# Optimization experiments

Hardware: AMD Instinct MI355X
Metric: run time of the kernel (lower is better)

## Reference

```python
import jax, jax.numpy as jnp
import numpy as np


def conv1x1(x, w, b):
    # x: [B,Ci,H,W], w: [Co,Ci,1,1], b: [Co]
    return jnp.einsum('bihw,oi->bohw', x, w[:, :, 0, 0]) + b[None, :, None, None]


def guide_nn(x, w1, b1, w2, b2):
    h = jax.nn.relu(conv1x1(x, w1, b1))
    return jnp.tanh(conv1x1(h, w2, b2))


def trilinear_slice(grid, gx, gy, gz):
    # grid: [B,C,D,Gh,Gw]; gx,gy,gz: [B,H,W] in ~[-1,1]
    B, C, D, Gh, Gw = grid.shape
    fx = jnp.clip((gx + 1.0) * 0.5 * (Gw - 1), 0.0, Gw - 1)
    fy = jnp.clip((gy + 1.0) * 0.5 * (Gh - 1), 0.0, Gh - 1)
    fz = jnp.clip((gz + 1.0) * 0.5 * (D - 1), 0.0, D - 1)
    x0 = jnp.floor(fx).astype(jnp.int32); x1 = jnp.minimum(x0 + 1, Gw - 1)
    y0 = jnp.floor(fy).astype(jnp.int32); y1 = jnp.minimum(y0 + 1, Gh - 1)
    z0 = jnp.floor(fz).astype(jnp.int32); z1 = jnp.minimum(z0 + 1, D - 1)
    wx = (fx - x0)[:, None]; wy = (fy - y0)[:, None]; wz = (fz - z0)[:, None]

    gather = jax.vmap(lambda g, zi, yi, xi: g[:, zi, yi, xi])  # -> [B,C,H,W]

    out = (
        gather(grid, z0, y0, x0) * (1 - wz) * (1 - wy) * (1 - wx)
        + gather(grid, z0, y0, x1) * (1 - wz) * (1 - wy) * wx
        + gather(grid, z0, y1, x0) * (1 - wz) * wy * (1 - wx)
        + gather(grid, z0, y1, x1) * (1 - wz) * wy * wx
        + gather(grid, z1, y0, x0) * wz * (1 - wy) * (1 - wx)
        + gather(grid, z1, y0, x1) * wz * (1 - wy) * wx
        + gather(grid, z1, y1, x0) * wz * wy * (1 - wx)
        + gather(grid, z1, y1, x1) * wz * wy * wx
    )
    return out


def slicing(grid, guide):
    # guide: [B,1,H,W] (single-channel context map)
    B, c, H, W = guide.shape
    x = (jnp.arange(W, dtype=guide.dtype) - W / 2) / (W / 2)
    y = (jnp.arange(H, dtype=guide.dtype) - H / 2) / (H / 2)
    yy, xx = jnp.meshgrid(y, x, indexing='ij')
    gx = jnp.broadcast_to(xx[None], (B, H, W))
    gy = jnp.broadcast_to(yy[None], (B, H, W))
    gz = guide[:, 0]
    return trilinear_slice(grid, gx, gy, gz)


def apply_coefficent(x, coeff):
    # x: [B,Ci,H,W]; coeff: [B,Co,Ci+1,H,W] -> per-pixel affine
    ci = x.shape[1]
    return jnp.einsum('boihw,bihw->bohw', coeff[:, :, :ci], x) + coeff[:, :, ci]


def setup_inputs() -> dict:
    key = jax.random.key(0)
    ks = jax.random.split(key, 12)
    B, H, W = 8, 512, 512
    D, Gh, Gw = 8, 16, 16
    inp = {
        'src': jax.random.uniform(ks[0], (B, 3, H, W), jnp.float32),
        'grid1': jax.random.normal(ks[1], (B, 32, D, Gh, Gw), jnp.float32),
        'grid2': jax.random.normal(ks[2], (B, 27, D, Gh, Gw), jnp.float32),
        'w1': jax.random.normal(ks[3], (16, 3, 1, 1), jnp.float32) * 0.1,
        'b1': jnp.zeros((16,), jnp.float32),
        'w2': jax.random.normal(ks[4], (1, 16, 1, 1), jnp.float32) * 0.1,
        'b2': jnp.zeros((1,), jnp.float32),
        'w3': jax.random.normal(ks[5], (16, 8, 1, 1), jnp.float32) * 0.1,
        'b3': jnp.zeros((16,), jnp.float32),
        'w4': jax.random.normal(ks[6], (1, 16, 1, 1), jnp.float32) * 0.1,
        'b4': jnp.zeros((1,), jnp.float32),
    }
    return inp


def reference(src, grid1, grid2, w1, b1, w2, b2, w3, b3, w4, b4):
    B, _, H, W = src.shape
    context_map = guide_nn(src, w1, b1, w2, b2)            # [B,1,H,W]
    coeff1 = slicing(grid1, context_map)                    # [B,32,H,W]
    coeff1_split = jnp.transpose(coeff1.reshape(B, 4, 8, H, W), (0, 2, 1, 3, 4))  # [B,8,4,H,W]
    hidden = jax.nn.relu(apply_coefficent(src, coeff1_split))  # [B,8,H,W]
    context_map2 = guide_nn(hidden, w3, b3, w4, b4)         # [B,1,H,W]
    coeff2 = slicing(grid2, context_map2)                   # [B,27,H,W]
    coeff2_split = jnp.transpose(coeff2.reshape(B, 9, 3, H, W), (0, 2, 1, 3, 4))  # [B,3,9,H,W]
    out = apply_coefficent(hidden, coeff2_split)            # [B,3,H,W]
    return out
```

## Files before the change

kernel.cpp:

```cpp
#include <hip/hip_runtime.h>
#include <math.h>

#define BATCH 8
#define IMH 512
#define IMW 512
#define HWSZ (IMH * IMW)
#define CH 32
#define CPADH 40
#define L_CELLS (16 * 8)
#define LSLOTH (L_CELLS * CPADH)

typedef _Float16 h1;
typedef _Float16 h2 __attribute__((ext_vector_type(2)));

union V16 {
    uint4 u;
    h2 h[4];
};

__device__ __forceinline__ float fast_tanh(float x) {
    float e = __expf(2.0f * x);
    return fmaf(-2.0f, __builtin_amdgcn_rcpf(e + 1.0f), 1.0f);
}
__device__ __forceinline__ unsigned packh(float a, float b) {
    h2 v;
    v[0] = (h1)a;
    v[1] = (h1)b;
    return __builtin_bit_cast(unsigned, v);
}
__device__ __forceinline__ h2 ash2(unsigned u) { return __builtin_bit_cast(h2, u); }
__device__ __forceinline__ h2 pkmax0(h2 v) { return __builtin_elementwise_max(v, (h2)(h1)0.0f); }


__global__ __launch_bounds__(256) void transpose_both(const float* __restrict__ g1,
                                                      const float* __restrict__ g2,
                                                      h1* __restrict__ t1,
                                                      h1* __restrict__ t2,
                                                      unsigned* __restrict__ wpk,
                                                      const float* __restrict__ w1,
                                                      const float* __restrict__ b1,
                                                      const float* __restrict__ w2,
                                                      const float* __restrict__ w3,
                                                      const float* __restrict__ b3,
                                                      const float* __restrict__ w4) {
    int idx = blockIdx.x * 256 + threadIdx.x;
    if (idx < 524288) {
        int x = idx & 15, y = (idx >> 4) & 15, z = (idx >> 8) & 7;
        int c = (idx >> 11) & 31, b = idx >> 16;
        t1[((((b * 16 + y) * 16 + x) * 8 + z) << 5) + c] = (h1)g1[idx];
    } else if (idx < 966656) {
        int j = idx - 524288;
        int x = j & 15, y = (j >> 4) & 15, z = (j >> 8) & 7;
        int r = j >> 11;
        int c = r % 27, b = r / 27;
        t2[((((b * 16 + y) * 16 + x) * 8 + z) << 5) + c] = (h1)g2[j];
    } else {
        int k = idx - 966656;
        int cell = k / 5, p = k - cell * 5;
        t2[(cell << 5) + 27 + p] = (h1)0.0f;
    }
    if (blockIdx.x == 4095) {
        int t = threadIdx.x;
        if (t < 24) {
            int i = t >> 3, n = t & 7;
            wpk[t] = packh(w1[2 * n * 3 + i], w1[(2 * n + 1) * 3 + i]);
        } else if (t < 32) {
            int n = t - 24;
            wpk[t] = packh(b1[2 * n], b1[2 * n + 1]);
        } else if (t < 40) {
            int n = t - 32;
            wpk[t] = packh(w2[2 * n], w2[2 * n + 1]);
        } else if (t < 104) {
            int k = t - 40;
            int n = k >> 3, i = k & 7;
            wpk[t] = packh(w3[2 * n * 8 + i], w3[(2 * n + 1) * 8 + i]);
        } else if (t < 112) {
            int n = t - 104;
            wpk[t] = packh(w4[2 * n], w4[2 * n + 1]);
        } else if (t < 120) {
            int n = t - 112;
            wpk[t] = packh(b3[2 * n], b3[2 * n + 1]);
        }
    }
}

template <bool TR>
__global__ __launch_bounds__(256, 4) void fused6(
    const float* __restrict__ src,
    const void* __restrict__ g1p,
    const void* __restrict__ g2p,
    const unsigned* __restrict__ wpk,
    const float* __restrict__ w1, const float* __restrict__ b1,
    const float* __restrict__ w2, const float* __restrict__ b2,
    const float* __restrict__ w3, const float* __restrict__ b3,
    const float* __restrict__ w4, const float* __restrict__ b4,
    float* __restrict__ out) {
    __shared__ __align__(16) h1 L1h[LSLOTH];
    __shared__ __align__(16) h1 L2h[LSLOTH];

    int tid = threadIdx.x;
    int h = blockIdx.x & 511;
    int b = blockIdx.x >> 9;

    float fy = (float)h * (15.0f / 512.0f);
    int y0 = (int)fy;
    float wy = fy - (float)y0;

    const float* sbase = src + (size_t)b * 3 * HWSZ + (size_t)h * IMW;
    float sA0 = sbase[tid],       sA1 = sbase[HWSZ + tid],       sA2 = sbase[2 * HWSZ + tid];
    float sB0 = sbase[tid + 256], sB1 = sbase[HWSZ + tid + 256], sB2 = sbase[2 * HWSZ + tid + 256];

    if (TR) {
        h2 wyh = (h2)(h1)wy;
        const uint4* p1 = (const uint4*)g1p + ((size_t)b * 16 + y0) * 512;
        const uint4* p2 = (const uint4*)g2p + ((size_t)b * 16 + y0) * 512;
#pragma unroll
        for (int t = tid; t < 512; t += 256) {
            int g = t & 3, cell = t >> 2;
            V16 v0, v1, r0;
            v0.u = p1[t];
            v1.u = p1[t + 512];
#pragma unroll
            for (int k = 0; k < 4; ++k) r0.h[k] = v0.h[k] + (v1.h[k] - v0.h[k]) * wyh;
            *(uint4*)&L1h[cell * CPADH + 8 * g] = r0.u;
            V16 u0, u1, r1;
            u0.u = p2[t];
            u1.u = p2[t + 512];
#pragma unroll
            for (int k = 0; k < 4; ++k) r1.h[k] = u0.h[k] + (u1.h[k] - u0.h[k]) * wyh;
            *(uint4*)&L2h[cell * CPADH + 8 * g] = r1.u;
        }
    } else {
        const float* g1f = (const float*)g1p;
        const float* g2f = (const float*)g2p;
        for (int t = tid; t < L_CELLS * CH; t += 256) {
            int c = t & 31, cell = t >> 5;
            int z = cell & 7, xj = cell >> 3;
            size_t o0 = ((((size_t)b * 32 + c) * 8 + z) * 16 + y0) * 16 + xj;
            float v0 = g1f[o0], v1 = g1f[o0 + 16];
            L1h[cell * CPADH + c] = (h1)fmaf(wy, v1 - v0, v0);
        }
        for (int t = tid; t < L_CELLS * CH; t += 256) {
            int c = t & 31, cell = t >> 5;
            int z = cell & 7, xj = cell >> 3;
            float v = 0.0f;
            if (c < 27) {
                size_t o0 = ((((size_t)b * 27 + c) * 8 + z) * 16 + y0) * 16 + xj;
                v = fmaf(wy, g2f[o0 + 16] - g2f[o0], g2f[o0]);
            }
            L2h[cell * CPADH + c] = (h1)v;
        }
    }
    __syncthreads();

    float* obase = out + (size_t)b * 3 * HWSZ + (size_t)h * IMW;
#pragma unroll 2
    for (int p = 0; p < 2; ++p) {
        int w = tid + (p << 8);
        float s0 = p ? sB0 : sA0;
        float s1 = p ? sB1 : sA1;
        float s2 = p ? sB2 : sA2;

        float acc;
        h2 s0h, s1h, s2h;
        if constexpr (TR) {
            s0h = (h2)(h1)s0;
            s1h = (h2)(h1)s1;
            s2h = (h2)(h1)s2;
            h2 A;
#pragma unroll
            for (int n = 0; n < 8; ++n) {
                h2 t = ash2(wpk[24 + n]);
                t += s0h * ash2(wpk[n]);
                t += s1h * ash2(wpk[8 + n]);
                t += s2h * ash2(wpk[16 + n]);
                t = pkmax0(t);
                if (n == 0) A = t * ash2(wpk[32]);
                else        A += t * ash2(wpk[32 + n]);
            }
            acc = b2[0] + (float)A[0] + (float)A[1];
        } else {
            acc = b2[0];
#pragma unroll
            for (int j = 0; j < 16; ++j) {
                float t = fmaf(w1[j * 3 + 0], s0,
                          fmaf(w1[j * 3 + 1], s1,
                          fmaf(w1[j * 3 + 2], s2, b1[j])));
                acc = fmaf(w2[j], fmaxf(t, 0.0f), acc);
            }
        }
        float fz = fmaf(fast_tanh(acc), 3.5f, 3.5f);
        fz = fminf(fmaxf(fz, 0.0f), 7.0f);
        int z0 = min((int)fz, 6);
        float wz = fz - (float)z0;

        float fx = (float)w * (15.0f / 512.0f);
        int x0 = (int)fx;
        float wx = fx - (float)x0;
        int a00 = (x0 * 8 + z0) * CPADH;

        float w11v = wx * wz;
        float w10v = wx - w11v;
        float w01v = wz - w11v;
        float w00v = 1.0f - wx - wz + w11v;
        h2 W00 = (h2)(h1)w00v, W01 = (h2)(h1)w01v, W10 = (h2)(h1)w10v, W11 = (h2)(h1)w11v;

        const uint4* p00 = (const uint4*)&L1h[a00];
        const uint4* p01 = (const uint4*)&L1h[a00 + CPADH];
        const uint4* p10 = (const uint4*)&L1h[a00 + 8 * CPADH];
        const uint4* p11 = (const uint4*)&L1h[a00 + 9 * CPADH];
        h2 c1h[16];
#pragma unroll
        for (int j = 0; j < 4; ++j) {
            V16 A, B, C, D;
            A.u = p00[j];
            B.u = p01[j];
            C.u = p10[j];
            D.u = p11[j];
#pragma unroll
            for (int k = 0; k < 4; ++k)
                c1h[j * 4 + k] = A.h[k] * W00 + B.h[k] * W01 + C.h[k] * W10 + D.h[k] * W11;
        }

        h2 hidh[4];
        float hidf[8];
        if constexpr (TR) {
#pragma unroll
            for (int n = 0; n < 4; ++n) {
                h2 t = c1h[12 + n];
                t += c1h[n] * s0h;
                t += c1h[4 + n] * s1h;
                t += c1h[8 + n] * s2h;
                hidh[n] = pkmax0(t);
                hidf[2 * n]     = (float)hidh[n][0];
                hidf[2 * n + 1] = (float)hidh[n][1];
            }
        } else {
#pragma unroll
            for (int o = 0; o < 8; ++o) {
                float t = fmaf((float)c1h[o >> 1][o & 1], s0,
                          fmaf((float)c1h[(8 + o) >> 1][o & 1], s1,
                          fmaf((float)c1h[(16 + o) >> 1][o & 1], s2,
                               (float)c1h[(24 + o) >> 1][o & 1])));
                hidf[o] = fmaxf(t, 0.0f);
            }
        }

        float acc2;
        if constexpr (TR) {
            h2 hs[8];
#pragma unroll
            for (int n = 0; n < 4; ++n) {
                hs[2 * n]     = (h2)hidh[n][0];
                hs[2 * n + 1] = (h2)hidh[n][1];
            }
            h2 A;
#pragma unroll
            for (int n = 0; n < 8; ++n) {
                h2 t = ash2(wpk[112 + n]);
#pragma unroll
                for (int i = 0; i < 8; ++i) t += hs[i] * ash2(wpk[40 + n * 8 + i]);
                t = pkmax0(t);
                if (n == 0) A = t * ash2(wpk[104]);
                else        A += t * ash2(wpk[104 + n]);
            }
            acc2 = b4[0] + (float)A[0] + (float)A[1];
        } else {
            acc2 = b4[0];
#pragma unroll
            for (int j = 0; j < 16; ++j) {
                float t = b3[j];
#pragma unroll
                for (int i = 0; i < 8; ++i) t = fmaf(w3[j * 8 + i], hidf[i], t);
                acc2 = fmaf(w4[j], fmaxf(t, 0.0f), acc2);
            }
        }
        float fz2 = fmaf(fast_tanh(acc2), 3.5f, 3.5f);
        fz2 = fminf(fmaxf(fz2, 0.0f), 7.0f);
        int z0b = min((int)fz2, 6);
        float wz2 = fz2 - (float)z0b;

        int a00b = (x0 * 8 + z0b) * CPADH;
        float u11 = wx * wz2;
        float u10 = wx - u11;
        float u01 = wz2 - u11;
        float u00 = 1.0f - wx - wz2 + u11;
        h2 U00 = (h2)(h1)u00, U01 = (h2)(h1)u01, U10 = (h2)(h1)u10, U11 = (h2)(h1)u11;

        const uint4* q00 = (const uint4*)&L2h[a00b];
        const uint4* q01 = (const uint4*)&L2h[a00b + CPADH];
        const uint4* q10 = (const uint4*)&L2h[a00b + 8 * CPADH];
        const uint4* q11 = (const uint4*)&L2h[a00b + 9 * CPADH];
        h2 c2h[14];
#pragma unroll
        for (int j = 0; j < 4; ++j) {
            V16 A, B, C, D;
            A.u = q00[j];
            B.u = q01[j];
            C.u = q10[j];
            D.u = q11[j];
#pragma unroll
            for (int k = 0; k < 4; ++k) {
                int m = j * 4 + k;
                if (m < 14)
                    c2h[m] = A.h[k] * U00 + B.h[k] * U01 + C.h[k] * U10 + D.h[k] * U11;
            }
        }

#pragma unroll
        for (int o = 0; o < 3; ++o) {
            float t = (float)c2h[(24 + o) >> 1][(24 + o) & 1];
#pragma unroll
            for (int i = 0; i < 8; ++i) {
                int c = i * 3 + o;
                t = fmaf((float)c2h[c >> 1][c & 1], hidf[i], t);
            }
            obase[(size_t)o * HWSZ + w] = t;
        }
    }
}

extern "C" void kernel_launch(void* const* d_in, const int* in_sizes, int n_in,
                              void* d_out, int out_size, void* d_ws, size_t ws_size,
                              hipStream_t stream) {
    const float* src   = (const float*)d_in[0];
    const float* grid1 = (const float*)d_in[1];
    const float* grid2 = (const float*)d_in[2];
    const float* w1 = (const float*)d_in[3];
    const float* b1 = (const float*)d_in[4];
    const float* w2 = (const float*)d_in[5];
    const float* b2 = (const float*)d_in[6];
    const float* w3 = (const float*)d_in[7];
    const float* b3 = (const float*)d_in[8];
    const float* w4 = (const float*)d_in[9];
    const float* b4 = (const float*)d_in[10];
    float* out = (float*)d_out;

    const size_t t_elems = (size_t)BATCH * 2048 * CH;
    const size_t ws_needed = 2 * t_elems * sizeof(h1) + 512;

    const int nblk = BATCH * IMH;

    if (ws_size >= ws_needed) {
        h1* t1 = (h1*)d_ws;
        h1* t2 = t1 + t_elems;
        unsigned* wpk = (unsigned*)(t2 + t_elems);
        transpose_both<<<4096, 256, 0, stream>>>(grid1, grid2, t1, t2, wpk,
                                                 w1, b1, w2, w3, b3, w4);
        fused6<true><<<nblk, 256, 0, stream>>>(
            src, t1, t2, wpk, w1, b1, w2, b2, w3, b3, w4, b4, out);
    } else {
        fused6<false><<<nblk, 256, 0, stream>>>(
            src, grid1, grid2, nullptr, w1, b1, w2, b2, w3, b3, w4, b4, out);
    }
}
```

Before: 121.9 us.

## Split each image row across two blocks with half-width grid staging

Each block now handles half a row (256 pixels, one per thread) and stages only the 9 x-cells of the y-interpolated bilateral grid that its half needs, instead of all 16. This halves LDS use per block, which allows a higher occupancy target in launch bounds, and doubles the grid size. The second-slice load now reads only the 27 used channels (3 uint4 plus one uint2 per corner). The hidf conversion moves after the second guide MLP. In exchange, the grid staging work for each row is partly repeated, since about 18 cells are loaded per row instead of 16, and each block does less work to amortize its setup.

Result: no change. 123.3 us (+1.1%).

```diff
diff --git a/kernel.cpp b/kernel.cpp
--- a/kernel.cpp
+++ b/kernel.cpp
@@ -7,8 +7,10 @@
 #define HWSZ (IMH * IMW)
 #define CH 32
 #define CPADH 40
-#define L_CELLS (16 * 8)
+#define XCELLS 9
+#define L_CELLS (XCELLS * 8)
 #define LSLOTH (L_CELLS * CPADH)
+#define NCHUNK (L_CELLS * 4)
 
 typedef _Float16 h1;
 typedef _Float16 h2 __attribute__((ext_vector_type(2)));
@@ -16,6 +18,10 @@
 union V16 {
     uint4 u;
     h2 h[4];
+};
+union V8 {
+    uint2 u;
+    h2 h[2];
 };
 
 __device__ __forceinline__ float fast_tanh(float x) {
@@ -85,7 +91,7 @@
 }
 
 template <bool TR>
-__global__ __launch_bounds__(256, 4) void fused6(
+__global__ __launch_bounds__(256, 8) void fused8(
     const float* __restrict__ src,
     const void* __restrict__ g1p,
     const void* __restrict__ g2p,
@@ -99,23 +105,27 @@
     __shared__ __align__(16) h1 L2h[LSLOTH];
 
     int tid = threadIdx.x;
-    int h = blockIdx.x & 511;
-    int b = blockIdx.x >> 9;
+    int gid = blockIdx.x;
+    int half = gid & 1;
+    int h = (gid >> 1) & 511;
+    int b = gid >> 10;
+    int xlo = half ? 7 : 0;
+    int w = (half << 8) + tid;
 
     float fy = (float)h * (15.0f / 512.0f);
     int y0 = (int)fy;
     float wy = fy - (float)y0;
 
     const float* sbase = src + (size_t)b * 3 * HWSZ + (size_t)h * IMW;
-    float sA0 = sbase[tid],       sA1 = sbase[HWSZ + tid],       sA2 = sbase[2 * HWSZ + tid];
-    float sB0 = sbase[tid + 256], sB1 = sbase[HWSZ + tid + 256], sB2 = sbase[2 * HWSZ + tid + 256];
+    float s0 = sbase[w];
+    float s1 = sbase[HWSZ + w];
+    float s2 = sbase[2 * HWSZ + w];
 
     if (TR) {
         h2 wyh = (h2)(h1)wy;
-        const uint4* p1 = (const uint4*)g1p + ((size_t)b * 16 + y0) * 512;
-        const uint4* p2 = (const uint4*)g2p + ((size_t)b * 16 + y0) * 512;
-#pragma unroll
-        for (int t = tid; t < 512; t += 256) {
+        const uint4* p1 = (const uint4*)g1p + ((size_t)b * 16 + y0) * 512 + xlo * 32;
+        const uint4* p2 = (const uint4*)g2p + ((size_t)b * 16 + y0) * 512 + xlo * 32;
+        for (int t = tid; t < NCHUNK; t += 256) {
             int g = t & 3, cell = t >> 2;
             V16 v0, v1, r0;
             v0.u = p1[t];
@@ -123,6 +133,9 @@
 #pragma unroll
             for (int k = 0; k < 4; ++k) r0.h[k] = v0.h[k] + (v1.h[k] - v0.h[k]) * wyh;
             *(uint4*)&L1h[cell * CPADH + 8 * g] = r0.u;
+        }
+        for (int t = tid; t < NCHUNK; t += 256) {
+            int g = t & 3, cell = t >> 2;
             V16 u0, u1, r1;
             u0.u = p2[t];
             u1.u = p2[t + 512];
@@ -135,14 +148,14 @@
         const float* g2f = (const float*)g2p;
         for (int t = tid; t < L_CELLS * CH; t += 256) {
             int c = t & 31, cell = t >> 5;
-            int z = cell & 7, xj = cell >> 3;
+            int z = cell & 7, xj = xlo + (cell >> 3);
             size_t o0 = ((((size_t)b * 32 + c) * 8 + z) * 16 + y0) * 16 + xj;
             float v0 = g1f[o0], v1 = g1f[o0 + 16];
             L1h[cell * CPADH + c] = (h1)fmaf(wy, v1 - v0, v0);
         }
         for (int t = tid; t < L_CELLS * CH; t += 256) {
             int c = t & 31, cell = t >> 5;
-            int z = cell & 7, xj = cell >> 3;
+            int z = cell & 7, xj = xlo + (cell >> 3);
             float v = 0.0f;
             if (c < 27) {
                 size_t o0 = ((((size_t)b * 27 + c) * 8 + z) * 16 + y0) * 16 + xj;
@@ -154,169 +167,172 @@
     __syncthreads();
 
     float* obase = out + (size_t)b * 3 * HWSZ + (size_t)h * IMW;
-#pragma unroll 2
-    for (int p = 0; p < 2; ++p) {
-        int w = tid + (p << 8);
-        float s0 = p ? sB0 : sA0;
-        float s1 = p ? sB1 : sA1;
-        float s2 = p ? sB2 : sA2;
-
-        float acc;
-        h2 s0h, s1h, s2h;
-        if constexpr (TR) {
-            s0h = (h2)(h1)s0;
-            s1h = (h2)(h1)s1;
-            s2h = (h2)(h1)s2;
-            h2 A;
-#pragma unroll
-            for (int n = 0; n < 8; ++n) {
-                h2 t = ash2(wpk[24 + n]);
-                t += s0h * ash2(wpk[n]);
-                t += s1h * ash2(wpk[8 + n]);
-                t += s2h * ash2(wpk[16 + n]);
-                t = pkmax0(t);
-                if (n == 0) A = t * ash2(wpk[32]);
-                else        A += t * ash2(wpk[32 + n]);
-            }
-            acc = b2[0] + (float)A[0] + (float)A[1];
-        } else {
-            acc = b2[0];
-#pragma unroll
-            for (int j = 0; j < 16; ++j) {
-                float t = fmaf(w1[j * 3 + 0], s0,
-                          fmaf(w1[j * 3 + 1], s1,
-                          fmaf(w1[j * 3 + 2], s2, b1[j])));
-                acc = fmaf(w2[j], fmaxf(t, 0.0f), acc);
-            }
-        }
-        float fz = fmaf(fast_tanh(acc), 3.5f, 3.5f);
-        fz = fminf(fmaxf(fz, 0.0f), 7.0f);
-        int z0 = min((int)fz, 6);
-        float wz = fz - (float)z0;
-
-        float fx = (float)w * (15.0f / 512.0f);
-        int x0 = (int)fx;
-        float wx = fx - (float)x0;
-        int a00 = (x0 * 8 + z0) * CPADH;
-
-        float w11v = wx * wz;
-        float w10v = wx - w11v;
-        float w01v = wz - w11v;
-        float w00v = 1.0f - wx - wz + w11v;
-        h2 W00 = (h2)(h1)w00v, W01 = (h2)(h1)w01v, W10 = (h2)(h1)w10v, W11 = (h2)(h1)w11v;
-
-        const uint4* p00 = (const uint4*)&L1h[a00];
-        const uint4* p01 = (const uint4*)&L1h[a00 + CPADH];
-        const uint4* p10 = (const uint4*)&L1h[a00 + 8 * CPADH];
-        const uint4* p11 = (const uint4*)&L1h[a00 + 9 * CPADH];
-        h2 c1h[16];
-#pragma unroll
-        for (int j = 0; j < 4; ++j) {
-            V16 A, B, C, D;
-            A.u = p00[j];
-            B.u = p01[j];
-            C.u = p10[j];
-            D.u = p11[j];
-#pragma unroll
-            for (int k = 0; k < 4; ++k)
-                c1h[j * 4 + k] = A.h[k] * W00 + B.h[k] * W01 + C.h[k] * W10 + D.h[k] * W11;
-        }
-
-        h2 hidh[4];
-        float hidf[8];
-        if constexpr (TR) {
-#pragma unroll
-            for (int n = 0; n < 4; ++n) {
-                h2 t = c1h[12 + n];
-                t += c1h[n] * s0h;
-                t += c1h[4 + n] * s1h;
-                t += c1h[8 + n] * s2h;
-                hidh[n] = pkmax0(t);
-                hidf[2 * n]     = (float)hidh[n][0];
-                hidf[2 * n + 1] = (float)hidh[n][1];
-            }
-        } else {
-#pragma unroll
-            for (int o = 0; o < 8; ++o) {
-                float t = fmaf((float)c1h[o >> 1][o & 1], s0,
-                          fmaf((float)c1h[(8 + o) >> 1][o & 1], s1,
-                          fmaf((float)c1h[(16 + o) >> 1][o & 1], s2,
-                               (float)c1h[(24 + o) >> 1][o & 1])));
-                hidf[o] = fmaxf(t, 0.0f);
-            }
-        }
-
-        float acc2;
-        if constexpr (TR) {
-            h2 hs[8];
-#pragma unroll
-            for (int n = 0; n < 4; ++n) {
-                hs[2 * n]     = (h2)hidh[n][0];
-                hs[2 * n + 1] = (h2)hidh[n][1];
-            }
-            h2 A;
-#pragma unroll
-            for (int n = 0; n < 8; ++n) {
-                h2 t = ash2(wpk[112 + n]);
-#pragma unroll
-                for (int i = 0; i < 8; ++i) t += hs[i] * ash2(wpk[40 + n * 8 + i]);
-                t = pkmax0(t);
-                if (n == 0) A = t * ash2(wpk[104]);
-                else        A += t * ash2(wpk[104 + n]);
-            }
-            acc2 = b4[0] + (float)A[0] + (float)A[1];
-        } else {
-            acc2 = b4[0];
-#pragma unroll
-            for (int j = 0; j < 16; ++j) {
-                float t = b3[j];
-#pragma unroll
-                for (int i = 0; i < 8; ++i) t = fmaf(w3[j * 8 + i], hidf[i], t);
-                acc2 = fmaf(w4[j], fmaxf(t, 0.0f), acc2);
-            }
-        }
-        float fz2 = fmaf(fast_tanh(acc2), 3.5f, 3.5f);
-        fz2 = fminf(fmaxf(fz2, 0.0f), 7.0f);
-        int z0b = min((int)fz2, 6);
-        float wz2 = fz2 - (float)z0b;
-
-        int a00b = (x0 * 8 + z0b) * CPADH;
-        float u11 = wx * wz2;
-        float u10 = wx - u11;
-        float u01 = wz2 - u11;
-        float u00 = 1.0f - wx - wz2 + u11;
-        h2 U00 = (h2)(h1)u00, U01 = (h2)(h1)u01, U10 = (h2)(h1)u10, U11 = (h2)(h1)u11;
-
-        const uint4* q00 = (const uint4*)&L2h[a00b];
-        const uint4* q01 = (const uint4*)&L2h[a00b + CPADH];
-        const uint4* q10 = (const uint4*)&L2h[a00b + 8 * CPADH];
-        const uint4* q11 = (const uint4*)&L2h[a00b + 9 * CPADH];
-        h2 c2h[14];
-#pragma unroll
-        for (int j = 0; j < 4; ++j) {
-            V16 A, B, C, D;
-            A.u = q00[j];
-            B.u = q01[j];
-            C.u = q10[j];
-            D.u = q11[j];
-#pragma unroll
-            for (int k = 0; k < 4; ++k) {
-                int m = j * 4 + k;
-                if (m < 14)
-                    c2h[m] = A.h[k] * U00 + B.h[k] * U01 + C.h[k] * U10 + D.h[k] * U11;
-            }
-        }
-
-#pragma unroll
-        for (int o = 0; o < 3; ++o) {
-            float t = (float)c2h[(24 + o) >> 1][(24 + o) & 1];
-#pragma unroll
-            for (int i = 0; i < 8; ++i) {
-                int c = i * 3 + o;
-                t = fmaf((float)c2h[c >> 1][c & 1], hidf[i], t);
-            }
-            obase[(size_t)o * HWSZ + w] = t;
-        }
+
+    float acc;
+    h2 s0h, s1h, s2h;
+    if constexpr (TR) {
+        s0h = (h2)(h1)s0;
+        s1h = (h2)(h1)s1;
+        s2h = (h2)(h1)s2;
+        h2 A;
+#pragma unroll
+        for (int n = 0; n < 8; ++n) {
+            h2 t = ash2(wpk[24 + n]);
+            t += s0h * ash2(wpk[n]);
+            t += s1h * ash2(wpk[8 + n]);
+            t += s2h * ash2(wpk[16 + n]);
+            t = pkmax0(t);
+            if (n == 0) A = t * ash2(wpk[32]);
+            else        A += t * ash2(wpk[32 + n]);
+        }
+        acc = b2[0] + (float)A[0] + (float)A[1];
+    } else {
+        acc = b2[0];
+#pragma unroll
+        for (int j = 0; j < 16; ++j) {
+            float t = fmaf(w1[j * 3 + 0], s0,
+                      fmaf(w1[j * 3 + 1], s1,
+                      fmaf(w1[j * 3 + 2], s2, b1[j])));
+            acc = fmaf(w2[j], fmaxf(t, 0.0f), acc);
+        }
+    }
+    float fz = fmaf(fast_tanh(acc), 3.5f, 3.5f);
+    fz = fminf(fmaxf(fz, 0.0f), 7.0f);
+    int z0 = min((int)fz, 6);
+    float wz = fz - (float)z0;
+
+    float fx = (float)w * (15.0f / 512.0f);
+    int x0 = (int)fx;
+    float wx = fx - (float)x0;
+    int a00 = ((x0 - xlo) * 8 + z0) * CPADH;
+
+    float w11v = wx * wz;
+    float w10v = wx - w11v;
+    float w01v = wz - w11v;
+    float w00v = 1.0f - wx - wz + w11v;
+    h2 W00 = (h2)(h1)w00v, W01 = (h2)(h1)w01v, W10 = (h2)(h1)w10v, W11 = (h2)(h1)w11v;
+
+    const uint4* p00 = (const uint4*)&L1h[a00];
+    const uint4* p01 = (const uint4*)&L1h[a00 + CPADH];
+    const uint4* p10 = (const uint4*)&L1h[a00 + 8 * CPADH];
+    const uint4* p11 = (const uint4*)&L1h[a00 + 9 * CPADH];
+    h2 c1h[16];
+#pragma unroll
+    for (int j = 0; j < 4; ++j) {
+        V16 A, B, C, D;
+        A.u = p00[j];
+        B.u = p01[j];
+        C.u = p10[j];
+        D.u = p11[j];
+#pragma unroll
+        for (int k = 0; k < 4; ++k)
+            c1h[j * 4 + k] = A.h[k] * W00 + B.h[k] * W01 + C.h[k] * W10 + D.h[k] * W11;
+    }
+
+    h2 hidh[4];
+    float hidf[8];
+    if constexpr (TR) {
+#pragma unroll
+        for (int n = 0; n < 4; ++n) {
+            h2 t = c1h[12 + n];
+            t += c1h[n] * s0h;
+            t += c1h[4 + n] * s1h;
+            t += c1h[8 + n] * s2h;
+            hidh[n] = pkmax0(t);
+        }
+    } else {
+#pragma unroll
+        for (int o = 0; o < 8; ++o) {
+            float t = fmaf((float)c1h[o >> 1][o & 1], s0,
+                      fmaf((float)c1h[(8 + o) >> 1][o & 1], s1,
+                      fmaf((float)c1h[(16 + o) >> 1][o & 1], s2,
+                           (float)c1h[(24 + o) >> 1][o & 1])));
+            hidf[o] = fmaxf(t, 0.0f);
+        }
+    }
+
+    float acc2;
+    if constexpr (TR) {
+        h2 hs[8];
+#pragma unroll
+        for (int n = 0; n < 4; ++n) {
+            hs[2 * n]     = (h2)hidh[n][0];
+            hs[2 * n + 1] = (h2)hidh[n][1];
+        }
+        h2 A;
+#pragma unroll
+        for (int n = 0; n < 8; ++n) {
+            h2 t = ash2(wpk[112 + n]);
+#pragma unroll
+            for (int i = 0; i < 8; ++i) t += hs[i] * ash2(wpk[40 + n * 8 + i]);
+            t = pkmax0(t);
+            if (n == 0) A = t * ash2(wpk[104]);
+            else        A += t * ash2(wpk[104 + n]);
+        }
+        acc2 = b4[0] + (float)A[0] + (float)A[1];
+#pragma unroll
+        for (int n = 0; n < 4; ++n) {
+            hidf[2 * n]     = (float)hidh[n][0];
+            hidf[2 * n + 1] = (float)hidh[n][1];
+        }
+    } else {
+        acc2 = b4[0];
+#pragma unroll
+        for (int j = 0; j < 16; ++j) {
+            float t = b3[j];
+#pragma unroll
+            for (int i = 0; i < 8; ++i) t = fmaf(w3[j * 8 + i], hidf[i], t);
+            acc2 = fmaf(w4[j], fmaxf(t, 0.0f), acc2);
+        }
+    }
+    float fz2 = fmaf(fast_tanh(acc2), 3.5f, 3.5f);
+    fz2 = fminf(fmaxf(fz2, 0.0f), 7.0f);
+    int z0b = min((int)fz2, 6);
+    float wz2 = fz2 - (float)z0b;
+
+    int a00b = ((x0 - xlo) * 8 + z0b) * CPADH;
+    float u11 = wx * wz2;
+    float u10 = wx - u11;
+    float u01 = wz2 - u11;
+    float u00 = 1.0f - wx - wz2 + u11;
+    h2 U00 = (h2)(h1)u00, U01 = (h2)(h1)u01, U10 = (h2)(h1)u10, U11 = (h2)(h1)u11;
+
+    const uint4* q00 = (const uint4*)&L2h[a00b];
+    const uint4* q01 = (const uint4*)&L2h[a00b + CPADH];
+    const uint4* q10 = (const uint4*)&L2h[a00b + 8 * CPADH];
+    const uint4* q11 = (const uint4*)&L2h[a00b + 9 * CPADH];
+    h2 c2h[14];
+#pragma unroll
+    for (int j = 0; j < 3; ++j) {
+        V16 A, B, C, D;
+        A.u = q00[j];
+        B.u = q01[j];
+        C.u = q10[j];
+        D.u = q11[j];
+#pragma unroll
+        for (int k = 0; k < 4; ++k)
+            c2h[j * 4 + k] = A.h[k] * U00 + B.h[k] * U01 + C.h[k] * U10 + D.h[k] * U11;
+    }
+    {
+        V8 A, B, C, D;
+        A.u = *(const uint2*)&L2h[a00b + 24];
+        B.u = *(const uint2*)&L2h[a00b + CPADH + 24];
+        C.u = *(const uint2*)&L2h[a00b + 8 * CPADH + 24];
+        D.u = *(const uint2*)&L2h[a00b + 9 * CPADH + 24];
+#pragma unroll
+        for (int k = 0; k < 2; ++k)
+            c2h[12 + k] = A.h[k] * U00 + B.h[k] * U01 + C.h[k] * U10 + D.h[k] * U11;
+    }
+
+#pragma unroll
+    for (int o = 0; o < 3; ++o) {
+        float t = (float)c2h[(24 + o) >> 1][(24 + o) & 1];
+#pragma unroll
+        for (int i = 0; i < 8; ++i) {
+            int c = i * 3 + o;
+            t = fmaf((float)c2h[c >> 1][c & 1], hidf[i], t);
+        }
+        obase[(size_t)o * HWSZ + w] = t;
     }
 }
 
@@ -339,7 +355,7 @@
     const size_t t_elems = (size_t)BATCH * 2048 * CH;
     const size_t ws_needed = 2 * t_elems * sizeof(h1) + 512;
 
-    const int nblk = BATCH * IMH;
+    const int nblk = BATCH * IMH * 2;
 
     if (ws_size >= ws_needed) {
         h1* t1 = (h1*)d_ws;
@@ -347,10 +363,10 @@
         unsigned* wpk = (unsigned*)(t2 + t_elems);
         transpose_both<<<4096, 256, 0, stream>>>(grid1, grid2, t1, t2, wpk,
                                                  w1, b1, w2, w3, b3, w4);
-        fused6<true><<<nblk, 256, 0, stream>>>(
+        fused8<true><<<nblk, 256, 0, stream>>>(
             src, t1, t2, wpk, w1, b1, w2, b2, w3, b3, w4, b4, out);
     } else {
-        fused6<false><<<nblk, 256, 0, stream>>>(
+        fused8<false><<<nblk, 256, 0, stream>>>(
             src, grid1, grid2, nullptr, w1, b1, w2, b2, w3, b3, w4, b4, out);
     }
 }
```
